# Kernel optimization log

Measured on AMD Instinct MI355X. Metric: run time of the kernel, lower is better.

## Reference

```python
import jax, jax.numpy as jnp
import numpy as np

DIM = 1024
NUM_HEADS = 16
HEAD_DIM = DIM // NUM_HEADS
BINDING_BIAS = 0.5
SCALE = HEAD_DIM ** -0.5


def setup_inputs() -> dict:
    key = jax.random.key(0)
    ks = jax.random.split(key, 10)
    B, S, D = 2, 2048, DIM
    std = D ** -0.5
    return {
        "x": jax.random.normal(ks[0], (B, S, D), jnp.float32),
        "binding_matrix": jax.random.uniform(ks[1], (S, S), jnp.float32),
        "Wq": jax.random.normal(ks[2], (D, D), jnp.float32) * std,
        "bq": jnp.zeros((D,), jnp.float32),
        "Wk": jax.random.normal(ks[3], (D, D), jnp.float32) * std,
        "bk": jnp.zeros((D,), jnp.float32),
        "Wv": jax.random.normal(ks[4], (D, D), jnp.float32) * std,
        "bv": jnp.zeros((D,), jnp.float32),
        "Wo": jax.random.normal(ks[5], (D, D), jnp.float32) * std,
        "bo": jnp.zeros((D,), jnp.float32),
    }


def reference(x, binding_matrix, Wq, bq, Wk, bk, Wv, bv, Wo, bo):
    B, S, D = x.shape
    H, Hd = NUM_HEADS, HEAD_DIM
    # projections -> [B, H, S, Hd]
    q = (x @ Wq + bq).reshape(B, S, H, Hd).transpose(0, 2, 1, 3)
    k = (x @ Wk + bk).reshape(B, S, H, Hd).transpose(0, 2, 1, 3)
    v = (x @ Wv + bv).reshape(B, S, H, Hd).transpose(0, 2, 1, 3)
    # scores [B, H, S, S] with additive binding bias
    attn = jnp.einsum("bhqd,bhkd->bhqk", q, k) * SCALE
    attn = attn + BINDING_BIAS * binding_matrix[None, None, :, :]
    attn = jax.nn.softmax(attn, axis=-1)
    out = jnp.einsum("bhqk,bhkd->bhqd", attn, v)
    out = out.transpose(0, 2, 1, 3).reshape(B, S, D)
    return out @ Wo + bo
```

## Files before the change

kernel.cpp:

```cpp
#include <hip/hip_runtime.h>

#define DEV static __device__ __forceinline__

typedef __attribute__((ext_vector_type(4))) float f32x4;
typedef __attribute__((ext_vector_type(8))) __bf16 bfv8;
typedef __attribute__((ext_vector_type(8))) short s8v;
typedef __attribute__((ext_vector_type(4))) short s4v;

DEV short f2bf(float f) {
    unsigned u = __float_as_uint(f);
    u = (u + 0x7fffu + ((u >> 16) & 1u)) >> 16;
    return (short)u;
}
DEV float bf2f(short s) { return __uint_as_float(((unsigned)(unsigned short)s) << 16); }

DEV void gload16(const void* g, void* l) {
    __builtin_amdgcn_global_load_lds(
        (const __attribute__((address_space(1))) void*)g,
        (__attribute__((address_space(3))) void*)l, 16, 0, 0);
}

DEV f32x4 mfma16(bfv8 a, bfv8 b, f32x4 c) {
    return __builtin_amdgcn_mfma_f32_16x16x32_bf16(a, b, c, 0, 0, 0);
}

DEV float max3f(float a, float b, float c) {
    float d;
    asm("v_max3_f32 %0, %1, %2, %3" : "=v"(d) : "v"(a), "v"(b), "v"(c));
    return d;
}
DEV unsigned cvtpk(float lo, float hi) {
    unsigned w;
    asm("v_cvt_pk_bf16_f32 %0, %1, %2" : "=v"(w) : "v"(lo), "v"(hi));
    return w;
}

DEV bfv8 ldsfrag(const short* base, int row, int slog) {
    int sp = slog ^ (row & 7);
    return *reinterpret_cast<const bfv8*>(base + row * 64 + sp * 8);
}

__global__ void k_cvt(const float* __restrict__ in, short* __restrict__ out, float s) {
    int i = blockIdx.x * blockDim.x + threadIdx.x;
    const float4* p = (const float4*)in + (size_t)i * 2;
    float4 a = p[0], b = p[1];
    s8v o;
    o[0] = f2bf(a.x * s); o[1] = f2bf(a.y * s); o[2] = f2bf(a.z * s); o[3] = f2bf(a.w * s);
    o[4] = f2bf(b.x * s); o[5] = f2bf(b.y * s); o[6] = f2bf(b.z * s); o[7] = f2bf(b.w * s);
    reinterpret_cast<s8v*>(out)[i] = o;
}

__global__ void k_cvtb(const float* __restrict__ in, short* __restrict__ out, float s) {
    int i = blockIdx.x * blockDim.x + threadIdx.x;
    int ktn = i >> 11, q = i & 2047;
    const float4* p = reinterpret_cast<const float4*>(in + (size_t)q * 2048 + ktn * 16);
    float4 a = p[0], b = p[1], cc = p[2], d = p[3];
    s8v o0, o1;
    o0[0] = f2bf(a.x * s); o0[1] = f2bf(a.y * s); o0[2] = f2bf(a.z * s); o0[3] = f2bf(a.w * s);
    o0[4] = f2bf(b.x * s); o0[5] = f2bf(b.y * s); o0[6] = f2bf(b.z * s); o0[7] = f2bf(b.w * s);
    o1[0] = f2bf(cc.x * s); o1[1] = f2bf(cc.y * s); o1[2] = f2bf(cc.z * s); o1[3] = f2bf(cc.w * s);
    o1[4] = f2bf(d.x * s); o1[5] = f2bf(d.y * s); o1[6] = f2bf(d.z * s); o1[7] = f2bf(d.w * s);
    s8v* dst = reinterpret_cast<s8v*>(out + (size_t)i * 16);
    dst[0] = o0; dst[1] = o1;
}

__global__ void k_transpose4(
    const float* __restrict__ W0, const float* __restrict__ W1,
    const float* __restrict__ W2, const float* __restrict__ W3,
    short* __restrict__ T0, short* __restrict__ T1,
    short* __restrict__ T2, short* __restrict__ T3, float s0)
{
    __shared__ float tl[32][33];
    const int z = blockIdx.z;
    const float* W = z == 0 ? W0 : z == 1 ? W1 : z == 2 ? W2 : W3;
    short* Wt = z == 0 ? T0 : z == 1 ? T1 : z == 2 ? T2 : T3;
    const float s = z == 0 ? s0 : 1.f;
    int tx = threadIdx.x & 31, ty = threadIdx.x >> 5;
    int nb = blockIdx.x * 32, kb = blockIdx.y * 32;
#pragma unroll
    for (int i = 0; i < 4; i++)
        tl[ty + i * 8][tx] = W[(kb + ty + i * 8) * 1024 + nb + tx];
    __syncthreads();
#pragma unroll
    for (int i = 0; i < 4; i++)
        Wt[(nb + ty + i * 8) * 1024 + kb + tx] = f2bf(tl[tx][ty + i * 8] * s);
}

template <int EPI>
DEV void gemm_store(f32x4 a4, int gr, int gc, const float* bias, float bscale,
                    void* outp)
{
    const float bvl = bias[gc] * bscale;
    const int h = gc >> 6, d = gc & 63;
    if (EPI == 2) {
        float* O = (float*)outp;
#pragma unroll
        for (int r = 0; r < 4; r++) O[(gr + r) * 1024 + gc] = a4[r] + bvl;
    } else {
        const int b = gr >> 11, sr = gr & 2047;
        short* O = (short*)outp;
        if (EPI == 0) {
            int base = ((b * 16 + h) * 2048 + sr) * 64 + d;
#pragma unroll
            for (int r = 0; r < 4; r++) O[base + r * 64] = f2bf(a4[r] + bvl);
        } else {
            s4v vv;
#pragma unroll
            for (int r = 0; r < 4; r++) vv[r] = f2bf(a4[r] + bvl);
            const int s6 = sr & 63;
            const int qp = (sr & ~63) | (s6 & 35) | ((s6 & 12) << 1) | ((s6 & 16) >> 2);
            *reinterpret_cast<s4v*>(O + ((b * 16 + h) * 64 + d) * 2048 + qp) = vv;
        }
    }
}

template <int EPI>
DEV void gemm_body(const short* __restrict__ A, const short* __restrict__ Bt,
                   const float* __restrict__ bias, void* __restrict__ outp,
                   float bscale, int row0, int col0, short (*As)[64 * 64],
                   short (*Bs)[128 * 64])
{
    const int t = threadIdx.x, lane = t & 63;
    const int wv = t >> 6, wr = wv >> 1, wc = wv & 1;
    const int g = lane >> 4, c = lane & 15;

    const f32x4 z4 = {0.f, 0.f, 0.f, 0.f};
    f32x4 acc[2][4];
#pragma unroll
    for (int m = 0; m < 2; m++)
#pragma unroll
        for (int n = 0; n < 4; n++) acc[m][n] = z4;

    const short* Ap[2]; const short* Bp[4]; int Ad[2], Bd[4];
#pragma unroll
    for (int j = 0; j < 2; j++) {
        int idx = j * 256 + t;
        int row = idx >> 3, sl = ((idx & 7) ^ (row & 7)) * 8;
        Ap[j] = A + row0 * 1024 + row * 1024 + sl;
        Ad[j] = idx * 8;
    }
#pragma unroll
    for (int j = 0; j < 4; j++) {
        int idx = j * 256 + t;
        int row = idx >> 3, sl = ((idx & 7) ^ (row & 7)) * 8;
        Bp[j] = Bt + col0 * 1024 + row * 1024 + sl;
        Bd[j] = idx * 8;
    }
    auto stage = [&](int buf) {
#pragma unroll
        for (int j = 0; j < 2; j++) { gload16(Ap[j], &As[buf][Ad[j]]); Ap[j] += 64; }
#pragma unroll
        for (int j = 0; j < 4; j++) { gload16(Bp[j], &Bs[buf][Bd[j]]); Bp[j] += 64; }
    };

    stage(0);
    __syncthreads();

    for (int kt = 0; kt < 16; ++kt) {
        const int cur = kt & 1;
        if (kt < 15) stage(cur ^ 1);

        bfv8 af[2][2], bfr[4][2];
#pragma unroll
        for (int m = 0; m < 2; m++)
#pragma unroll
            for (int ks = 0; ks < 2; ks++)
                af[m][ks] = ldsfrag(As[cur], wr * 32 + m * 16 + c, ks * 4 + g);
#pragma unroll
        for (int n = 0; n < 4; n++)
#pragma unroll
            for (int ks = 0; ks < 2; ks++)
                bfr[n][ks] = ldsfrag(Bs[cur], wc * 64 + n * 16 + c, ks * 4 + g);
        __builtin_amdgcn_s_setprio(1);
#pragma unroll
        for (int m = 0; m < 2; m++)
#pragma unroll
            for (int n = 0; n < 4; n++)
#pragma unroll
                for (int ks = 0; ks < 2; ks++)
                    acc[m][n] = mfma16(af[m][ks], bfr[n][ks], acc[m][n]);
        __builtin_amdgcn_s_setprio(0);
        __syncthreads();
    }

#pragma unroll
    for (int n = 0; n < 4; n++) {
        const int gc = col0 + wc * 64 + n * 16 + c;
#pragma unroll
        for (int m = 0; m < 2; m++)
            gemm_store<EPI>(acc[m][n], row0 + wr * 32 + m * 16 + g * 4, gc,
                            bias, bscale, outp);
    }
}

template <int EPI>
DEV void gemm_body128(const short* __restrict__ A, const short* __restrict__ Bt,
                      const float* __restrict__ bias, void* __restrict__ outp,
                      float bscale, int row0, int col0, short (*As)[128 * 64],
                      short (*Bs)[128 * 64])
{
    const int t = threadIdx.x, lane = t & 63;
    const int wv = t >> 6, wr = wv >> 1, wc = wv & 1;
    const int g = lane >> 4, c = lane & 15;

    const f32x4 z4 = {0.f, 0.f, 0.f, 0.f};
    f32x4 acc[4][4];
#pragma unroll
    for (int m = 0; m < 4; m++)
#pragma unroll
        for (int n = 0; n < 4; n++) acc[m][n] = z4;

    const short* Ap[4]; const short* Bp[4]; int Cd[4];
#pragma unroll
    for (int j = 0; j < 4; j++) {
        int idx = j * 256 + t;
        int row = idx >> 3, sl = ((idx & 7) ^ (row & 7)) * 8;
        Ap[j] = A + row0 * 1024 + row * 1024 + sl;
        Bp[j] = Bt + col0 * 1024 + row * 1024 + sl;
        Cd[j] = idx * 8;
    }
    auto stage = [&](int buf) {
#pragma unroll
        for (int j = 0; j < 4; j++) {
            gload16(Ap[j], &As[buf][Cd[j]]); Ap[j] += 64;
            gload16(Bp[j], &Bs[buf][Cd[j]]); Bp[j] += 64;
        }
    };

    stage(0);
    __syncthreads();

    for (int kt = 0; kt < 16; ++kt) {
        const int cur = kt & 1;
        if (kt < 15) stage(cur ^ 1);

        bfv8 af[4][2], bfr[4][2];
#pragma unroll
        for (int m = 0; m < 4; m++)
#pragma unroll
            for (int ks = 0; ks < 2; ks++)
                af[m][ks] = ldsfrag(As[cur], wr * 64 + m * 16 + c, ks * 4 + g);
#pragma unroll
        for (int n = 0; n < 4; n++)
#pragma unroll
            for (int ks = 0; ks < 2; ks++)
                bfr[n][ks] = ldsfrag(Bs[cur], wc * 64 + n * 16 + c, ks * 4 + g);
        __builtin_amdgcn_s_setprio(1);
#pragma unroll
        for (int m = 0; m < 4; m++)
#pragma unroll
            for (int n = 0; n < 4; n++)
#pragma unroll
                for (int ks = 0; ks < 2; ks++)
                    acc[m][n] = mfma16(af[m][ks], bfr[n][ks], acc[m][n]);
        __builtin_amdgcn_s_setprio(0);
        __syncthreads();
    }

#pragma unroll
    for (int n = 0; n < 4; n++) {
        const int gc = col0 + wc * 64 + n * 16 + c;
#pragma unroll
        for (int m = 0; m < 4; m++)
            gemm_store<EPI>(acc[m][n], row0 + wr * 64 + m * 16 + g * 4, gc,
                            bias, bscale, outp);
    }
}

__global__ __launch_bounds__(256, 2) void k_gemm3(
    const short* __restrict__ A,
    const short* __restrict__ WqT, const short* __restrict__ WkT, const short* __restrict__ WvT,
    const float* __restrict__ bq, const float* __restrict__ bk, const float* __restrict__ bv,
    short* __restrict__ Qs, short* __restrict__ Kst, short* __restrict__ Vts, float scq)
{
    __shared__ alignas(16) short As[2][128 * 64];
    __shared__ alignas(16) short Bs[2][128 * 64];
    const int which = blockIdx.y >> 3;
    const int col0 = (blockIdx.y & 7) * 128;
    const int row0 = blockIdx.x * 128;
    if (which == 0)
        gemm_body128<0>(A, WqT, bq, Qs, scq, row0, col0, As, Bs);
    else if (which == 1)
        gemm_body128<0>(A, WkT, bk, Kst, 1.f, row0, col0, As, Bs);
    else
        gemm_body128<1>(A, WvT, bv, Vts, 1.f, row0, col0, As, Bs);
}

__global__ __launch_bounds__(256, 2) void k_gemmO(
    const short* __restrict__ A, const short* __restrict__ Bt,
    const float* __restrict__ bias, float* __restrict__ outp)
{
    __shared__ alignas(16) short As[2][64 * 64];
    __shared__ alignas(16) short Bs[2][128 * 64];
    gemm_body<2>(A, Bt, bias, outp, 1.f, blockIdx.x * 64, blockIdx.y * 128, As, Bs);
}

__global__ __launch_bounds__(1024, 4) void k_attn(
    const short* __restrict__ Q, const short* __restrict__ K,
    const short* __restrict__ Vt, const short* __restrict__ bbt,
    short* __restrict__ Ob)
{
    __shared__ alignas(16) short Ks[2][64 * 64];
    __shared__ alignas(16) short Vs[2][64 * 64];
    const int t = threadIdx.x, lane = t & 63;
    const int wv = t >> 6, g = lane >> 4, c = lane & 15;
    const int qt = blockIdx.x, bh = blockIdx.y;
    const int b = bh >> 4, h = bh & 15;
    const short* Qb = Q + bh * 2048 * 64;
    const short* Kb = K + bh * 2048 * 64;
    const short* Vb = Vt + bh * 64 * 2048;
    const int q0 = qt * 256 + wv * 16;

    bfv8 qf[2];
#pragma unroll
    for (int ks = 0; ks < 2; ks++)
        qf[ks] = *reinterpret_cast<const bfv8*>(Qb + (q0 + c) * 64 + ks * 32 + g * 8);

    const f32x4 z4 = {0.f, 0.f, 0.f, 0.f};
    f32x4 oa[4];
#pragma unroll
    for (int nd = 0; nd < 4; nd++) oa[nd] = z4;
    f32x4 lacc = z4;
    float mrun = 20.0f;

    s8v ob_;
#pragma unroll
    for (int i = 0; i < 8; i++) ob_[i] = (short)0x3F80;
    const bfv8 ones = __builtin_bit_cast(bfv8, ob_);

    const bool isK = t < 512;
    const int sidx = isK ? t : t - 512;
    const int srow = sidx >> 3, ssl = ((sidx & 7) ^ (srow & 7)) * 8;
    const short* sp_ = isK ? (Kb + srow * 64 + ssl) : (Vb + srow * 2048 + ssl);
    const int sinc = isK ? 4096 : 64;
    const int dst8 = sidx * 8;
    const short* bbp = bbt + (size_t)(q0 + c) * 16 + 4 * g;

    const int cx = c & 7;
    const int fofs0 = c * 128 + ((g ^ cx) << 4);
    const int fofs1 = c * 128 + (((4 + g) ^ cx) << 4);

    gload16(sp_, isK ? &Ks[0][dst8] : &Vs[0][dst8]);
    sp_ += sinc;
    s4v bn[4];
#pragma unroll
    for (int n = 0; n < 4; n++)
        bn[n] = *reinterpret_cast<const s4v*>(bbp + n * 32768);
    bbp += 131072;
    __syncthreads();

    for (int kt = 0; kt < 32; ++kt) {
        const int cur = kt & 1;
        f32x4 cb[4];
#pragma unroll
        for (int n = 0; n < 4; n++)
#pragma unroll
            for (int r = 0; r < 4; r++) cb[n][r] = bf2f(bn[n][r]);
        if (kt < 31) {
            const int nb = cur ^ 1;
            gload16(sp_, isK ? &Ks[nb][dst8] : &Vs[nb][dst8]);
            sp_ += sinc;
#pragma unroll
            for (int n = 0; n < 4; n++)
                bn[n] = *reinterpret_cast<const s4v*>(bbp + n * 32768);
            bbp += 131072;
        }

        const char* Kc = (const char*)&Ks[cur][0];
        const char* Vc = (const char*)&Vs[cur][0];

        f32x4 sc[4];
        __builtin_amdgcn_s_setprio(1);
#pragma unroll
        for (int n = 0; n < 4; n++) {
            bfv8 k0 = *reinterpret_cast<const bfv8*>(Kc + fofs0 + n * 2048);
            bfv8 k1 = *reinterpret_cast<const bfv8*>(Kc + fofs1 + n * 2048);
            sc[n] = mfma16(k0, qf[0], cb[n]);
            sc[n] = mfma16(k1, qf[1], sc[n]);
        }
        __builtin_amdgcn_s_setprio(0);

#pragma unroll
        for (int n = 0; n < 4; n++)
#pragma unroll
            for (int r = 0; r < 4; r++)
                sc[n][r] = __builtin_amdgcn_exp2f(sc[n][r] - mrun);

        unsigned w0[4], w1[4];
#pragma unroll
        for (int n = 0; n < 4; n++) {
            w0[n] = cvtpk(sc[n][0], sc[n][1]);
            w1[n] = cvtpk(sc[n][2], sc[n][3]);
        }
        typedef struct { unsigned a, b, c2, d; } u4;
        u4 q0w; q0w.a = w0[0]; q0w.b = w1[0]; q0w.c2 = w0[1]; q0w.d = w1[1];
        u4 q1w; q1w.a = w0[2]; q1w.b = w1[2]; q1w.c2 = w0[3]; q1w.d = w1[3];
        const bfv8 pf0 = __builtin_bit_cast(bfv8, q0w);
        const bfv8 pf1 = __builtin_bit_cast(bfv8, q1w);

        __builtin_amdgcn_s_setprio(1);
#pragma unroll
        for (int nd = 0; nd < 4; nd++) {
            bfv8 v0 = *reinterpret_cast<const bfv8*>(Vc + fofs0 + nd * 2048);
            bfv8 v1 = *reinterpret_cast<const bfv8*>(Vc + fofs1 + nd * 2048);
            oa[nd] = mfma16(v0, pf0, oa[nd]);
            oa[nd] = mfma16(v1, pf1, oa[nd]);
        }
        lacc = mfma16(ones, pf0, lacc);
        lacc = mfma16(ones, pf1, lacc);
        __builtin_amdgcn_s_setprio(0);

        float t0 = fmaxf(max3f(sc[0][0], sc[0][1], sc[0][2]), sc[0][3]);
        float t1 = fmaxf(max3f(sc[1][0], sc[1][1], sc[1][2]), sc[1][3]);
        float t2 = fmaxf(max3f(sc[2][0], sc[2][1], sc[2][2]), sc[2][3]);
        float t3 = fmaxf(max3f(sc[3][0], sc[3][1], sc[3][2]), sc[3][3]);
        float pemax = fmaxf(max3f(t0, t1, t2), t3);
        if (!__all(pemax <= 2896.0f)) {
            float rmax = fmaxf(pemax, __shfl_xor(pemax, 16));
            rmax = fmaxf(rmax, __shfl_xor(rmax, 32));
            if (rmax > 2896.0f) {
                const float corr = 1.0f / rmax;
                mrun += __log2f(rmax);
#pragma unroll
                for (int nd = 0; nd < 4; nd++)
#pragma unroll
                    for (int r = 0; r < 4; r++) oa[nd][r] *= corr;
#pragma unroll
                for (int r = 0; r < 4; r++) lacc[r] *= corr;
            }
        }
        __syncthreads();
    }

    const float rl = 1.0f / lacc[0];
    const size_t orow = (size_t)(b * 2048 + q0 + c);
#pragma unroll
    for (int nd = 0; nd < 4; nd++) {
        s4v st;
#pragma unroll
        for (int r = 0; r < 4; r++) st[r] = f2bf(oa[nd][r] * rl);
        *reinterpret_cast<s4v*>(Ob + orow * 1024 + h * 64 + nd * 16 + 4 * g) = st;
    }
}

extern "C" void kernel_launch(void* const* d_in, const int* in_sizes, int n_in,
                              void* d_out, int out_size, void* d_ws, size_t ws_size,
                              hipStream_t stream)
{
    (void)in_sizes; (void)n_in; (void)out_size; (void)ws_size;
    const float* x    = (const float*)d_in[0];
    const float* bind = (const float*)d_in[1];
    const float* Wq   = (const float*)d_in[2];
    const float* bq   = (const float*)d_in[3];
    const float* Wk   = (const float*)d_in[4];
    const float* bk   = (const float*)d_in[5];
    const float* Wv   = (const float*)d_in[6];
    const float* bv   = (const float*)d_in[7];
    const float* Wo   = (const float*)d_in[8];
    const float* bo   = (const float*)d_in[9];

    char* ws = (char*)d_ws;
    const size_t MB = (size_t)1 << 20;
    short* xb   = (short*)(ws + 0 * MB);
    short* Wqt  = (short*)(ws + 8 * MB);
    short* Wkt  = (short*)(ws + 10 * MB);
    short* Wvt  = (short*)(ws + 12 * MB);
    short* Wot  = (short*)(ws + 14 * MB);
    short* bbm  = (short*)(ws + 16 * MB);
    short* Qs   = (short*)(ws + 24 * MB);
    short* Kst  = (short*)(ws + 32 * MB);
    short* Vts  = (short*)(ws + 40 * MB);
    short* Obuf = (short*)(ws + 48 * MB);

    const float LOG2E = 1.4426950408889634f;
    const float SCQ = 0.125f * LOG2E;
    const float SCB = 0.5f * LOG2E;

    k_cvt<<<2048, 256, 0, stream>>>(x, xb, 1.f);
    k_cvtb<<<1024, 256, 0, stream>>>(bind, bbm, SCB);
    k_transpose4<<<dim3(32, 32, 4), 256, 0, stream>>>(Wq, Wk, Wv, Wo,
                                                      Wqt, Wkt, Wvt, Wot, SCQ);
    k_gemm3<<<dim3(32, 24), 256, 0, stream>>>(xb, Wqt, Wkt, Wvt, bq, bk, bv,
                                              Qs, Kst, Vts, SCQ);
    k_attn<<<dim3(8, 32), 1024, 0, stream>>>(Qs, Kst, Vts, bbm, Obuf);
    k_gemmO<<<dim3(64, 8), 256, 0, stream>>>(Obuf, Wot, bo, (float*)d_out);
}
```

Baseline: 123.4 us.

## Switch attention to 32x32x16 MFMA tiles with 512-thread blocks

The attention kernel moves from 16x16x32 to 32x32x16 bf16 MFMA. Each wave now owns 32 query rows, so a block is 8 waves of 512 threads instead of 16 waves of 1024, and every thread stages both K and V tiles. The bias-matrix pre-layout kernel is rewritten as an LDS-tiled transpose into 8-wide key groups to match the new fragment layout, and the V permutation in the QKV epilogue is adjusted to match. The goal is fewer MFMA issues and fragment loads per unit of work and better LDS reuse per wave; the cost is larger accumulators per wave (register pressure) and half as many waves resident to hide latency.

```diff
diff --git a/kernel.cpp b/kernel.cpp
--- a/kernel.cpp
+++ b/kernel.cpp
@@ -3,6 +3,7 @@
 #define DEV static __device__ __forceinline__
 
 typedef __attribute__((ext_vector_type(4))) float f32x4;
+typedef __attribute__((ext_vector_type(16))) float f32x16;
 typedef __attribute__((ext_vector_type(8))) __bf16 bfv8;
 typedef __attribute__((ext_vector_type(8))) short s8v;
 typedef __attribute__((ext_vector_type(4))) short s4v;
@@ -22,6 +23,9 @@
 
 DEV f32x4 mfma16(bfv8 a, bfv8 b, f32x4 c) {
     return __builtin_amdgcn_mfma_f32_16x16x32_bf16(a, b, c, 0, 0, 0);
+}
+DEV f32x16 mfma32(bfv8 a, bfv8 b, f32x16 c) {
+    return __builtin_amdgcn_mfma_f32_32x32x16_bf16(a, b, c, 0, 0, 0);
 }
 
 DEV float max3f(float a, float b, float c) {
@@ -51,17 +55,30 @@
 }
 
 __global__ void k_cvtb(const float* __restrict__ in, short* __restrict__ out, float s) {
-    int i = blockIdx.x * blockDim.x + threadIdx.x;
-    int ktn = i >> 11, q = i & 2047;
-    const float4* p = reinterpret_cast<const float4*>(in + (size_t)q * 2048 + ktn * 16);
-    float4 a = p[0], b = p[1], cc = p[2], d = p[3];
-    s8v o0, o1;
-    o0[0] = f2bf(a.x * s); o0[1] = f2bf(a.y * s); o0[2] = f2bf(a.z * s); o0[3] = f2bf(a.w * s);
-    o0[4] = f2bf(b.x * s); o0[5] = f2bf(b.y * s); o0[6] = f2bf(b.z * s); o0[7] = f2bf(b.w * s);
-    o1[0] = f2bf(cc.x * s); o1[1] = f2bf(cc.y * s); o1[2] = f2bf(cc.z * s); o1[3] = f2bf(cc.w * s);
-    o1[4] = f2bf(d.x * s); o1[5] = f2bf(d.y * s); o1[6] = f2bf(d.z * s); o1[7] = f2bf(d.w * s);
-    s8v* dst = reinterpret_cast<s8v*>(out + (size_t)i * 16);
-    dst[0] = o0; dst[1] = o1;
+    __shared__ float tl[64][68];
+    const int t = threadIdx.x;
+    const int q0 = blockIdx.x * 64, c0 = blockIdx.y * 64;
+    {
+        int row = t >> 2, ch = t & 3;
+        const float* src = in + (size_t)(q0 + row) * 2048 + c0 + ch * 16;
+        float* dst = &tl[row][ch * 16];
+#pragma unroll
+        for (int j = 0; j < 4; j++) {
+            float4 v = reinterpret_cast<const float4*>(src)[j];
+            dst[4 * j + 0] = v.x; dst[4 * j + 1] = v.y;
+            dst[4 * j + 2] = v.z; dst[4 * j + 3] = v.w;
+        }
+    }
+    __syncthreads();
+    const int c8 = t >> 5, qq = t & 31;
+#pragma unroll
+    for (int half = 0; half < 2; half++) {
+        int q = qq + 32 * half;
+        s8v o;
+#pragma unroll
+        for (int v = 0; v < 8; v++) o[v] = f2bf(tl[q][c8 * 8 + v] * s);
+        *reinterpret_cast<s8v*>(out + ((size_t)((c0 >> 3) + c8) * 2048 + q0 + q) * 8) = o;
+    }
 }
 
 __global__ void k_transpose4(
@@ -108,7 +125,7 @@
 #pragma unroll
             for (int r = 0; r < 4; r++) vv[r] = f2bf(a4[r] + bvl);
             const int s6 = sr & 63;
-            const int qp = (sr & ~63) | (s6 & 35) | ((s6 & 12) << 1) | ((s6 & 16) >> 2);
+            const int qp = (sr & ~63) | (s6 & 51) | ((s6 & 4) << 1) | ((s6 & 8) >> 1);
             *reinterpret_cast<s4v*>(O + ((b * 16 + h) * 64 + d) * 2048 + qp) = vv;
         }
     }
@@ -295,7 +312,7 @@
     gemm_body<2>(A, Bt, bias, outp, 1.f, blockIdx.x * 64, blockIdx.y * 128, As, Bs);
 }
 
-__global__ __launch_bounds__(1024, 4) void k_attn(
+__global__ __launch_bounds__(512, 1) void k_attn(
     const short* __restrict__ Q, const short* __restrict__ K,
     const short* __restrict__ Vt, const short* __restrict__ bbt,
     short* __restrict__ Ob)
@@ -303,24 +320,28 @@
     __shared__ alignas(16) short Ks[2][64 * 64];
     __shared__ alignas(16) short Vs[2][64 * 64];
     const int t = threadIdx.x, lane = t & 63;
-    const int wv = t >> 6, g = lane >> 4, c = lane & 15;
+    const int wv = t >> 6, qr = lane & 31, hi = lane >> 5;
     const int qt = blockIdx.x, bh = blockIdx.y;
     const int b = bh >> 4, h = bh & 15;
     const short* Qb = Q + bh * 2048 * 64;
     const short* Kb = K + bh * 2048 * 64;
     const short* Vb = Vt + bh * 64 * 2048;
-    const int q0 = qt * 256 + wv * 16;
-
-    bfv8 qf[2];
-#pragma unroll
-    for (int ks = 0; ks < 2; ks++)
-        qf[ks] = *reinterpret_cast<const bfv8*>(Qb + (q0 + c) * 64 + ks * 32 + g * 8);
-
-    const f32x4 z4 = {0.f, 0.f, 0.f, 0.f};
-    f32x4 oa[4];
-#pragma unroll
-    for (int nd = 0; nd < 4; nd++) oa[nd] = z4;
-    f32x4 lacc = z4;
+    const int q0 = qt * 256 + wv * 32;
+    const int qg = q0 + qr;
+
+    bfv8 qf[4];
+#pragma unroll
+    for (int ks = 0; ks < 4; ks++)
+        qf[ks] = *reinterpret_cast<const bfv8*>(Qb + qg * 64 + 16 * ks + 8 * hi);
+
+    f32x16 oa[2];
+#pragma unroll
+    for (int dt = 0; dt < 2; dt++)
+#pragma unroll
+        for (int r = 0; r < 16; r++) oa[dt][r] = 0.f;
+    f32x16 lacc;
+#pragma unroll
+    for (int r = 0; r < 16; r++) lacc[r] = 0.f;
     float mrun = 20.0f;
 
     s8v ob_;
@@ -328,119 +349,134 @@
     for (int i = 0; i < 8; i++) ob_[i] = (short)0x3F80;
     const bfv8 ones = __builtin_bit_cast(bfv8, ob_);
 
-    const bool isK = t < 512;
-    const int sidx = isK ? t : t - 512;
-    const int srow = sidx >> 3, ssl = ((sidx & 7) ^ (srow & 7)) * 8;
-    const short* sp_ = isK ? (Kb + srow * 64 + ssl) : (Vb + srow * 2048 + ssl);
-    const int sinc = isK ? 4096 : 64;
-    const int dst8 = sidx * 8;
-    const short* bbp = bbt + (size_t)(q0 + c) * 16 + 4 * g;
-
-    const int cx = c & 7;
-    const int fofs0 = c * 128 + ((g ^ cx) << 4);
-    const int fofs1 = c * 128 + (((4 + g) ^ cx) << 4);
-
-    gload16(sp_, isK ? &Ks[0][dst8] : &Vs[0][dst8]);
-    sp_ += sinc;
-    s4v bn[4];
-#pragma unroll
-    for (int n = 0; n < 4; n++)
-        bn[n] = *reinterpret_cast<const s4v*>(bbp + n * 32768);
+    const int srow = t >> 3, ssl = ((t & 7) ^ (srow & 7)) * 8;
+    const short* kp = Kb + srow * 64 + ssl;
+    const short* vp = Vb + srow * 2048 + ssl;
+    const int dst8 = t * 8;
+    const short* bbp = bbt + (size_t)qg * 8 + 4 * hi;
+
+    const int qx = qr & 7;
+    int ofs[2][4];
+#pragma unroll
+    for (int tt = 0; tt < 2; tt++)
+#pragma unroll
+        for (int ks = 0; ks < 4; ks++)
+            ofs[tt][ks] = (32 * tt + qr) * 128 + (((2 * ks + hi) ^ qx) << 4);
+
+    gload16(kp, &Ks[0][dst8]);
+    gload16(vp, &Vs[0][dst8]);
+    kp += 4096; vp += 64;
+    s4v bn[8];
+#pragma unroll
+    for (int g8 = 0; g8 < 8; g8++)
+        bn[g8] = *reinterpret_cast<const s4v*>(bbp + g8 * 16384);
     bbp += 131072;
     __syncthreads();
 
     for (int kt = 0; kt < 32; ++kt) {
         const int cur = kt & 1;
-        f32x4 cb[4];
-#pragma unroll
-        for (int n = 0; n < 4; n++)
-#pragma unroll
-            for (int r = 0; r < 4; r++) cb[n][r] = bf2f(bn[n][r]);
+        f32x16 sc0, sc1;
+#pragma unroll
+        for (int u = 0; u < 4; u++)
+#pragma unroll
+            for (int v = 0; v < 4; v++) {
+                sc0[4 * u + v] = bf2f(bn[u][v]);
+                sc1[4 * u + v] = bf2f(bn[4 + u][v]);
+            }
         if (kt < 31) {
             const int nb = cur ^ 1;
-            gload16(sp_, isK ? &Ks[nb][dst8] : &Vs[nb][dst8]);
-            sp_ += sinc;
-#pragma unroll
-            for (int n = 0; n < 4; n++)
-                bn[n] = *reinterpret_cast<const s4v*>(bbp + n * 32768);
+            gload16(kp, &Ks[nb][dst8]);
+            gload16(vp, &Vs[nb][dst8]);
+            kp += 4096; vp += 64;
+#pragma unroll
+            for (int g8 = 0; g8 < 8; g8++)
+                bn[g8] = *reinterpret_cast<const s4v*>(bbp + g8 * 16384);
             bbp += 131072;
         }
 
         const char* Kc = (const char*)&Ks[cur][0];
         const char* Vc = (const char*)&Vs[cur][0];
 
-        f32x4 sc[4];
         __builtin_amdgcn_s_setprio(1);
 #pragma unroll
-        for (int n = 0; n < 4; n++) {
-            bfv8 k0 = *reinterpret_cast<const bfv8*>(Kc + fofs0 + n * 2048);
-            bfv8 k1 = *reinterpret_cast<const bfv8*>(Kc + fofs1 + n * 2048);
-            sc[n] = mfma16(k0, qf[0], cb[n]);
-            sc[n] = mfma16(k1, qf[1], sc[n]);
-        }
+        for (int ks = 0; ks < 4; ks++)
+            sc0 = mfma32(*reinterpret_cast<const bfv8*>(Kc + ofs[0][ks]), qf[ks], sc0);
+#pragma unroll
+        for (int ks = 0; ks < 4; ks++)
+            sc1 = mfma32(*reinterpret_cast<const bfv8*>(Kc + ofs[1][ks]), qf[ks], sc1);
         __builtin_amdgcn_s_setprio(0);
 
 #pragma unroll
-        for (int n = 0; n < 4; n++)
-#pragma unroll
-            for (int r = 0; r < 4; r++)
-                sc[n][r] = __builtin_amdgcn_exp2f(sc[n][r] - mrun);
-
-        unsigned w0[4], w1[4];
-#pragma unroll
-        for (int n = 0; n < 4; n++) {
-            w0[n] = cvtpk(sc[n][0], sc[n][1]);
-            w1[n] = cvtpk(sc[n][2], sc[n][3]);
-        }
+        for (int r = 0; r < 16; r++) {
+            sc0[r] = __builtin_amdgcn_exp2f(sc0[r] - mrun);
+            sc1[r] = __builtin_amdgcn_exp2f(sc1[r] - mrun);
+        }
+
         typedef struct { unsigned a, b, c2, d; } u4;
-        u4 q0w; q0w.a = w0[0]; q0w.b = w1[0]; q0w.c2 = w0[1]; q0w.d = w1[1];
-        u4 q1w; q1w.a = w0[2]; q1w.b = w1[2]; q1w.c2 = w0[3]; q1w.d = w1[3];
-        const bfv8 pf0 = __builtin_bit_cast(bfv8, q0w);
-        const bfv8 pf1 = __builtin_bit_cast(bfv8, q1w);
+        bfv8 pf[4];
+#pragma unroll
+        for (int m = 0; m < 2; m++) {
+            u4 w0, w1;
+            w0.a = cvtpk(sc0[8 * m + 0], sc0[8 * m + 1]);
+            w0.b = cvtpk(sc0[8 * m + 2], sc0[8 * m + 3]);
+            w0.c2 = cvtpk(sc0[8 * m + 4], sc0[8 * m + 5]);
+            w0.d = cvtpk(sc0[8 * m + 6], sc0[8 * m + 7]);
+            pf[m] = __builtin_bit_cast(bfv8, w0);
+            w1.a = cvtpk(sc1[8 * m + 0], sc1[8 * m + 1]);
+            w1.b = cvtpk(sc1[8 * m + 2], sc1[8 * m + 3]);
+            w1.c2 = cvtpk(sc1[8 * m + 4], sc1[8 * m + 5]);
+            w1.d = cvtpk(sc1[8 * m + 6], sc1[8 * m + 7]);
+            pf[2 + m] = __builtin_bit_cast(bfv8, w1);
+        }
 
         __builtin_amdgcn_s_setprio(1);
 #pragma unroll
-        for (int nd = 0; nd < 4; nd++) {
-            bfv8 v0 = *reinterpret_cast<const bfv8*>(Vc + fofs0 + nd * 2048);
-            bfv8 v1 = *reinterpret_cast<const bfv8*>(Vc + fofs1 + nd * 2048);
-            oa[nd] = mfma16(v0, pf0, oa[nd]);
-            oa[nd] = mfma16(v1, pf1, oa[nd]);
-        }
-        lacc = mfma16(ones, pf0, lacc);
-        lacc = mfma16(ones, pf1, lacc);
+        for (int dt = 0; dt < 2; dt++)
+#pragma unroll
+            for (int cs = 0; cs < 4; cs++)
+                oa[dt] = mfma32(*reinterpret_cast<const bfv8*>(Vc + ofs[dt][cs]),
+                                pf[cs], oa[dt]);
+#pragma unroll
+        for (int cs = 0; cs < 4; cs++)
+            lacc = mfma32(ones, pf[cs], lacc);
         __builtin_amdgcn_s_setprio(0);
 
-        float t0 = fmaxf(max3f(sc[0][0], sc[0][1], sc[0][2]), sc[0][3]);
-        float t1 = fmaxf(max3f(sc[1][0], sc[1][1], sc[1][2]), sc[1][3]);
-        float t2 = fmaxf(max3f(sc[2][0], sc[2][1], sc[2][2]), sc[2][3]);
-        float t3 = fmaxf(max3f(sc[3][0], sc[3][1], sc[3][2]), sc[3][3]);
-        float pemax = fmaxf(max3f(t0, t1, t2), t3);
+        float p0 = 0.f, p1 = 0.f;
+#pragma unroll
+        for (int u = 0; u < 4; u++) {
+            p0 = fmaxf(p0, fmaxf(max3f(sc0[4 * u], sc0[4 * u + 1], sc0[4 * u + 2]),
+                                 sc0[4 * u + 3]));
+            p1 = fmaxf(p1, fmaxf(max3f(sc1[4 * u], sc1[4 * u + 1], sc1[4 * u + 2]),
+                                 sc1[4 * u + 3]));
+        }
+        float pemax = fmaxf(p0, p1);
         if (!__all(pemax <= 2896.0f)) {
-            float rmax = fmaxf(pemax, __shfl_xor(pemax, 16));
-            rmax = fmaxf(rmax, __shfl_xor(rmax, 32));
+            float rmax = fmaxf(pemax, __shfl_xor(pemax, 32));
             if (rmax > 2896.0f) {
                 const float corr = 1.0f / rmax;
                 mrun += __log2f(rmax);
 #pragma unroll
-                for (int nd = 0; nd < 4; nd++)
-#pragma unroll
-                    for (int r = 0; r < 4; r++) oa[nd][r] *= corr;
-#pragma unroll
-                for (int r = 0; r < 4; r++) lacc[r] *= corr;
+                for (int dt = 0; dt < 2; dt++)
+#pragma unroll
+                    for (int r = 0; r < 16; r++) oa[dt][r] *= corr;
+#pragma unroll
+                for (int r = 0; r < 16; r++) lacc[r] *= corr;
             }
         }
         __syncthreads();
     }
 
     const float rl = 1.0f / lacc[0];
-    const size_t orow = (size_t)(b * 2048 + q0 + c);
-#pragma unroll
-    for (int nd = 0; nd < 4; nd++) {
-        s4v st;
-#pragma unroll
-        for (int r = 0; r < 4; r++) st[r] = f2bf(oa[nd][r] * rl);
-        *reinterpret_cast<s4v*>(Ob + orow * 1024 + h * 64 + nd * 16 + 4 * g) = st;
-    }
+    short* Op = Ob + (size_t)(b * 2048 + qg) * 1024 + h * 64 + 4 * hi;
+#pragma unroll
+    for (int dt = 0; dt < 2; dt++)
+#pragma unroll
+        for (int u = 0; u < 4; u++) {
+            s4v st;
+#pragma unroll
+            for (int v = 0; v < 4; v++) st[v] = f2bf(oa[dt][4 * u + v] * rl);
+            *reinterpret_cast<s4v*>(Op + 32 * dt + 8 * u) = st;
+        }
 }
 
 extern "C" void kernel_launch(void* const* d_in, const int* in_sizes, int n_in,
@@ -477,11 +513,11 @@
     const float SCB = 0.5f * LOG2E;
 
     k_cvt<<<2048, 256, 0, stream>>>(x, xb, 1.f);
-    k_cvtb<<<1024, 256, 0, stream>>>(bind, bbm, SCB);
+    k_cvtb<<<dim3(32, 32), 256, 0, stream>>>(bind, bbm, SCB);
     k_transpose4<<<dim3(32, 32, 4), 256, 0, stream>>>(Wq, Wk, Wv, Wo,
                                                       Wqt, Wkt, Wvt, Wot, SCQ);
     k_gemm3<<<dim3(32, 24), 256, 0, stream>>>(xb, Wqt, Wkt, Wvt, bq, bk, bv,
                                               Qs, Kst, Vts, SCQ);
-    k_attn<<<dim3(8, 32), 1024, 0, stream>>>(Qs, Kst, Vts, bbm, Obuf);
+    k_attn<<<dim3(8, 32), 512, 0, stream>>>(Qs, Kst, Vts, bbm, Obuf);
     k_gemmO<<<dim3(64, 8), 256, 0, stream>>>(Obuf, Wot, bo, (float*)d_out);
 }
```

New measurement: 138.3 us. 1.12x slower.
